# Kernel tuning notes

Hardware: AMD Instinct MI355X
Metric: run time of the kernel (lower is better)

The kernel has to match this reference:

```python
import jax, jax.numpy as jnp
import numpy as np
import math

GROUPS = 32
HEADS = 8
EPS = 1e-5


def group_norm(x, w, b):
    B, C, H, W = x.shape
    xg = x.reshape(B, GROUPS, C // GROUPS, H, W)
    mu = xg.mean(axis=(2, 3, 4), keepdims=True)
    var = xg.var(axis=(2, 3, 4), keepdims=True)
    xg = (xg - mu) * jax.lax.rsqrt(var + EPS)
    return xg.reshape(B, C, H, W) * w[None, :, None, None] + b[None, :, None, None]


def setup_inputs() -> dict:
    key = jax.random.key(0)
    ks = jax.random.split(key, 3)
    C = 512
    x = jax.random.normal(ks[0], (4, C, 64, 64), dtype=jnp.float32)
    norm_w = jnp.ones((C,), dtype=jnp.float32)
    norm_b = jnp.zeros((C,), dtype=jnp.float32)
    qkv_w = jax.random.normal(ks[1], (3 * C, C), dtype=jnp.float32) * 0.02
    qkv_b = jnp.zeros((3 * C,), dtype=jnp.float32)
    proj_w = jax.random.normal(ks[2], (C, C), dtype=jnp.float32) * 0.02
    proj_b = jnp.zeros((C,), dtype=jnp.float32)
    return {"x": x, "norm_w": norm_w, "norm_b": norm_b, "qkv_w": qkv_w,
            "qkv_b": qkv_b, "proj_w": proj_w, "proj_b": proj_b}


def reference(x, norm_w, norm_b, qkv_w, qkv_b, proj_w, proj_b):
    B, C, H, W = x.shape
    S = H * W
    head_dim = C // HEADS
    scale = 1.0 / math.sqrt(head_dim)

    h = group_norm(x, norm_w, norm_b)
    # 1x1 conv == pointwise linear over channels
    qkv = jnp.einsum('oc,bchw->bohw', qkv_w, h) + qkv_b[None, :, None, None]
    q, k, v = jnp.split(qkv, 3, axis=1)
    q = q.reshape(B, HEADS, head_dim, S)
    k = k.reshape(B, HEADS, head_dim, S)
    v = v.reshape(B, HEADS, head_dim, S)

    # chunked softmax attention in the original is row-wise softmax, i.e.
    # mathematically identical to full attention over all queries
    attn = jnp.einsum('bhdi,bhdj->bhij', q, k) * scale  # [B,H,S,S]
    attn = jax.nn.softmax(attn, axis=-1)
    out = jnp.einsum('bhij,bhdj->bhdi', attn, v)  # [B,H,d,S]

    out = out.reshape(B, C, H, W)
    out = jnp.einsum('oc,bchw->bohw', proj_w, out) + proj_b[None, :, None, None]
    return out + x
```

## Files before the change

kernel.cpp:

```cpp
#include <hip/hip_runtime.h>
#include <hip/hip_bf16.h>

#define NB 4
#define NC 512
#define NS 4096
#define NH 8
#define HD 64
#define NG 32
#define CPG 16
#define QKC 1024
#define CQF 0.18033688f

typedef __attribute__((ext_vector_type(8))) short bf16x8;
typedef __attribute__((ext_vector_type(4))) float f32x4;
typedef __attribute__((ext_vector_type(16))) float f32x16;

__device__ __forceinline__ unsigned short f2bf(float f) {
  union { float f; unsigned int u; } v; v.f = f;
  unsigned int r = v.u + 0x7FFFu + ((v.u >> 16) & 1u);
  return (unsigned short)(r >> 16);
}

__device__ __forceinline__ unsigned short f2bf_rn(float f) {
  union { __hip_bfloat16 h; unsigned short u; } cv;
  cv.h = __float2bfloat16(f);
  return cv.u;
}

__device__ __forceinline__ void gload16(const unsigned short* g, unsigned short* s) {
  __builtin_amdgcn_global_load_lds(
      (const __attribute__((address_space(1))) unsigned int*)g,
      (__attribute__((address_space(3))) unsigned int*)s, 16, 0, 0);
}

__global__ __launch_bounds__(256) void wprep_k(const float* __restrict__ wq,
                                               const float* __restrict__ wp,
                                               unsigned short* __restrict__ wqb,
                                               unsigned short* __restrict__ wpb,
                                               int nq8, int np8, int scale_end8) {
  int i = blockIdx.x * 256 + threadIdx.x;
  if (i >= nq8 + np8) return;
  const float* src;
  unsigned short* dst;
  float sc;
  int j;
  if (i < nq8) { src = wq; dst = wqb; j = i; sc = (i < scale_end8) ? CQF : 1.0f; }
  else         { src = wp; dst = wpb; j = i - nq8; sc = 1.0f; }
  const float4* s = (const float4*)src + (size_t)j * 2;
  float4 a = s[0], b = s[1];
  ushort4 u0 = make_ushort4(f2bf_rn(a.x * sc), f2bf_rn(a.y * sc),
                            f2bf_rn(a.z * sc), f2bf_rn(a.w * sc));
  ushort4 u1 = make_ushort4(f2bf_rn(b.x * sc), f2bf_rn(b.y * sc),
                            f2bf_rn(b.z * sc), f2bf_rn(b.w * sc));
  uint4 o;
  o.x = (unsigned)u0.x | ((unsigned)u0.y << 16);
  o.y = (unsigned)u0.z | ((unsigned)u0.w << 16);
  o.z = (unsigned)u1.x | ((unsigned)u1.y << 16);
  o.w = (unsigned)u1.z | ((unsigned)u1.w << 16);
  *((uint4*)dst + j) = o;
}

__global__ __launch_bounds__(256) void gn_stats_k(const float* __restrict__ x,
                                                  float* __restrict__ pstats) {
  int bgq = blockIdx.x;
  const float4* xp = (const float4*)(x + (size_t)bgq * (CPG * NS / 4));
  float s = 0.f, s2 = 0.f;
  #pragma unroll 4
  for (int i = threadIdx.x; i < CPG * NS / 16; i += 256) {
    float4 v = xp[i];
    s  += v.x + v.y + v.z + v.w;
    s2 += v.x * v.x + v.y * v.y + v.z * v.z + v.w * v.w;
  }
  #pragma unroll
  for (int off = 32; off > 0; off >>= 1) {
    s  += __shfl_down(s, off);
    s2 += __shfl_down(s2, off);
  }
  __shared__ float rs[4], rs2[4];
  int wid = threadIdx.x >> 6;
  if ((threadIdx.x & 63) == 0) { rs[wid] = s; rs2[wid] = s2; }
  __syncthreads();
  if (threadIdx.x == 0) {
    pstats[bgq * 2]     = rs[0] + rs[1] + rs[2] + rs[3];
    pstats[bgq * 2 + 1] = rs2[0] + rs2[1] + rs2[2] + rs2[3];
  }
}

__global__ __launch_bounds__(256) void gn_apply_k(const float* __restrict__ x,
                                                  const float* __restrict__ pstats,
                                                  const float* __restrict__ nw,
                                                  const float* __restrict__ nb,
                                                  unsigned short* __restrict__ ht) {
  int st = blockIdx.x, ct = blockIdx.y, b = blockIdx.z;
  int c0 = ct * 64, s0 = st * 64;
  __shared__ unsigned short lds[64][72];
  for (int idx = threadIdx.x; idx < 1024; idx += 256) {
    int row = idx >> 4, c4 = idx & 15;
    int c = c0 + row;
    int gi = (b * NG + (c >> 4)) * 4;
    const float4* pq = (const float4*)(pstats + gi * 2);
    float4 p01 = pq[0], p23 = pq[1];
    float sum = p01.x + p01.z + p23.x + p23.z;
    float ssq = p01.y + p01.w + p23.y + p23.w;
    float inv_n = 1.0f / (CPG * NS);
    float mu = sum * inv_n;
    float var = ssq * inv_n - mu * mu;
    float rstd = rsqrtf(var + 1e-5f);
    float sw = nw[c] * rstd;
    float sb = nb[c] - mu * sw;
    float4 v = *(const float4*)(x + ((size_t)b * NC + c) * NS + s0 + c4 * 4);
    ushort4 u = make_ushort4(f2bf(v.x * sw + sb), f2bf(v.y * sw + sb),
                             f2bf(v.z * sw + sb), f2bf(v.w * sw + sb));
    *(ushort4*)&lds[row][c4 * 4] = u;
  }
  __syncthreads();
  for (int idx = threadIdx.x; idx < 1024; idx += 256) {
    int i = idx >> 4, ch = idx & 15;
    ushort4 u = make_ushort4(lds[ch * 4 + 0][i], lds[ch * 4 + 1][i],
                             lds[ch * 4 + 2][i], lds[ch * 4 + 3][i]);
    *(ushort4*)(ht + ((size_t)b * NS + s0 + i) * NC + c0 + ch * 4) = u;
  }
}

__global__ __launch_bounds__(256) void qkv_gemm_k(const unsigned short* __restrict__ ht,
                                                  const unsigned short* __restrict__ wqb,
                                                  const float* __restrict__ bq,
                                                  unsigned short* __restrict__ qk,
                                                  unsigned short* __restrict__ vt) {
  int b = blockIdx.z;
  int m0 = blockIdx.x * 128, n0 = blockIdx.y * 128;
  __shared__ unsigned short alds[128 * 64];
  __shared__ unsigned short blds[128 * 64];
  const unsigned short* A = ht + (size_t)b * NS * NC;
  int tid = threadIdx.x;
  int l = tid & 63, w = tid >> 6;
  int wr = w >> 1, wc = w & 1;
  int lm = l & 15, lg = l >> 4;
  int lrow = l >> 3, lcb = l & 7;
  f32x4 acc[4][4];
  #pragma unroll
  for (int mi = 0; mi < 4; mi++)
    #pragma unroll
    for (int ni = 0; ni < 4; ni++) acc[mi][ni] = (f32x4){0.f, 0.f, 0.f, 0.f};

  for (int k0 = 0; k0 < NC; k0 += 64) {
    #pragma unroll
    for (int j = 0; j < 4; j++) {
      int row = w * 32 + j * 8 + lrow;
      int scb = lcb ^ (row & 7);
      gload16(A   + (size_t)(m0 + row) * NC + k0 + scb * 8, &alds[(w * 4 + j) * 512]);
      gload16(wqb + (size_t)(n0 + row) * NC + k0 + scb * 8, &blds[(w * 4 + j) * 512]);
    }
    __syncthreads();
    #pragma unroll
    for (int ks = 0; ks < 2; ks++) {
      bf16x8 af[4], bfr[4];
      #pragma unroll
      for (int mi = 0; mi < 4; mi++) {
        int row = wr * 64 + mi * 16 + lm;
        af[mi] = *(const bf16x8*)&alds[((row << 6) + (ks << 5) + (lg << 3)) ^ ((row & 7) << 3)];
      }
      #pragma unroll
      for (int ni = 0; ni < 4; ni++) {
        int row = wc * 64 + ni * 16 + lm;
        bfr[ni] = *(const bf16x8*)&blds[((row << 6) + (ks << 5) + (lg << 3)) ^ ((row & 7) << 3)];
      }
      #pragma unroll
      for (int mi = 0; mi < 4; mi++)
        #pragma unroll
        for (int ni = 0; ni < 4; ni++)
          acc[mi][ni] = __builtin_amdgcn_mfma_f32_16x16x32_bf16(af[mi], bfr[ni], acc[mi][ni], 0, 0, 0);
    }
    __syncthreads();
  }
  if (n0 < QKC) {
    #pragma unroll
    for (int mi = 0; mi < 4; mi++) {
      #pragma unroll
      for (int ni = 0; ni < 4; ni++) {
        int o = n0 + wc * 64 + ni * 16 + lm;
        float bias = bq[o];
        if (o < NC) bias *= CQF;
        #pragma unroll
        for (int q = 0; q < 4; q++) {
          int s = m0 + wr * 64 + mi * 16 + lg * 4 + q;
          qk[((size_t)b * NS + s) * QKC + o] = f2bf(acc[mi][ni][q] + bias);
        }
      }
    }
  } else {
    #pragma unroll
    for (int mi = 0; mi < 4; mi++) {
      int s0 = m0 + wr * 64 + mi * 16 + lg * 4;
      #pragma unroll
      for (int ni = 0; ni < 4; ni++) {
        int o = n0 + wc * 64 + ni * 16 + lm;
        float bias = bq[o];
        int dg = o - QKC;
        ushort4 u = make_ushort4(f2bf(acc[mi][ni][0] + bias), f2bf(acc[mi][ni][1] + bias),
                                 f2bf(acc[mi][ni][2] + bias), f2bf(acc[mi][ni][3] + bias));
        *(ushort4*)(vt + ((size_t)b * NC + dg) * NS + s0) = u;
      }
    }
  }
}

__global__ __launch_bounds__(256) void attn_k(const unsigned short* __restrict__ qk,
                                              const unsigned short* __restrict__ vt,
                                              unsigned short* __restrict__ ob) {
  int qt = blockIdx.x, h = blockIdx.y, b = blockIdx.z;
  int tid = threadIdx.x;
  int l = tid & 63, w = tid >> 6;
  int l31 = l & 31, hi = l >> 5;
  __shared__ unsigned short slds[16384];
  const unsigned short* qkb = qk + (size_t)b * NS * QKC;
  const unsigned short* vtb = vt + ((size_t)b * NC + h * HD) * NS;
  int iw = qt * 128 + w * 32;

  bf16x8 fq[4];
  #pragma unroll
  for (int kk = 0; kk < 4; kk++)
    fq[kk] = *(const bf16x8*)(qkb + (size_t)(iw + l31) * QKC + h * HD + kk * 16 + hi * 8);

  bf16x8 ones;
  #pragma unroll
  for (int e = 0; e < 8; e++) ones[e] = (short)0x3F80;

  int rb = (((l31 << 6) + (hi << 3)) ^ ((l31 & 7) << 3));
  int rbk[4] = { rb, rb ^ 16, rb ^ 32, rb ^ 48 };

  int sr = tid >> 3, sch = (tid & 7) * 8;
  const unsigned short* kp0 = qkb + NC + h * HD + (size_t)sr * QKC + sch;
  const unsigned short* kp1 = kp0 + (size_t)32 * QKC;
  const unsigned short* vp0 = vtb + (size_t)sr * NS + sch;
  const unsigned short* vp1 = vp0 + (size_t)32 * NS;
  int dk0 = (((sr << 6) + sch) ^ ((sr & 7) << 3));
  int dk1 = ((((sr + 32) << 6) + sch) ^ ((sr & 7) << 3));

  f32x16 acc_o0 = {}, acc_o1 = {}, acc_l = {};

  bf16x8 vA[8], vB[8], pA[4], pB[4];
  #pragma unroll
  for (int e = 0; e < 8; e++) vB[e] = (bf16x8){0, 0, 0, 0, 0, 0, 0, 0};
  #pragma unroll
  for (int e = 0; e < 4; e++) pB[e] = (bf16x8){0, 0, 0, 0, 0, 0, 0, 0};

  uint4 rk0 = *(const uint4*)kp0, rk1 = *(const uint4*)kp1;
  uint4 rv0 = *(const uint4*)vp0, rv1 = *(const uint4*)vp1;
  *(uint4*)&slds[dk0] = rk0;        *(uint4*)&slds[dk1] = rk1;
  *(uint4*)&slds[4096 + dk0] = rv0; *(uint4*)&slds[4096 + dk1] = rv1;
  kp0 += (size_t)64 * QKC; kp1 += (size_t)64 * QKC; vp0 += 64; vp1 += 64;
  rk0 = *(const uint4*)kp0; rk1 = *(const uint4*)kp1;
  rv0 = *(const uint4*)vp0; rv1 = *(const uint4*)vp1;
  __syncthreads();

  #define CVTSW(SA, q, DST) {                                                       \
    unsigned X0, X1, Y0, Y1;                                                        \
    asm("v_cvt_pk_bf16_f32 %0, %1, %2" : "=v"(X0) : "v"(SA[q*8+0]), "v"(SA[q*8+1]));\
    asm("v_cvt_pk_bf16_f32 %0, %1, %2" : "=v"(X1) : "v"(SA[q*8+2]), "v"(SA[q*8+3]));\
    asm("v_cvt_pk_bf16_f32 %0, %1, %2" : "=v"(Y0) : "v"(SA[q*8+4]), "v"(SA[q*8+5]));\
    asm("v_cvt_pk_bf16_f32 %0, %1, %2" : "=v"(Y1) : "v"(SA[q*8+6]), "v"(SA[q*8+7]));\
    asm("v_permlane32_swap_b32 %0, %1" : "+v"(X0), "+v"(Y0));                       \
    asm("v_permlane32_swap_b32 %0, %1" : "+v"(X1), "+v"(Y1));                       \
    union { unsigned u[4]; bf16x8 v; } pu = {{X0, X1, Y0, Y1}};                     \
    DST = pu.v; }

  #define TILE(BUF, t, VN, VP, PN, PP) {                                            \
    *(uint4*)&slds[(BUF^1)*8192 + dk0] = rk0;                                       \
    *(uint4*)&slds[(BUF^1)*8192 + dk1] = rk1;                                       \
    *(uint4*)&slds[(BUF^1)*8192 + 4096 + dk0] = rv0;                                \
    *(uint4*)&slds[(BUF^1)*8192 + 4096 + dk1] = rv1;                                \
    if ((t) + 2 < 64) {                                                             \
      kp0 += (size_t)64 * QKC; kp1 += (size_t)64 * QKC; vp0 += 64; vp1 += 64;       \
      rk0 = *(const uint4*)kp0; rk1 = *(const uint4*)kp1;                           \
      rv0 = *(const uint4*)vp0; rv1 = *(const uint4*)vp1;                           \
    }                                                                               \
    const unsigned short* Kr = &slds[(BUF)*8192];                                   \
    const unsigned short* Vr = &slds[(BUF)*8192 + 4096];                            \
    f32x16 sa0 = {}, sa1 = {};                                                      \
    __builtin_amdgcn_s_setprio(1);                                                  \
    _Pragma("unroll")                                                               \
    for (int kk = 0; kk < 4; kk++) {                                                \
      bf16x8 ak = *(const bf16x8*)&Kr[rbk[kk]];                                     \
      sa0 = __builtin_amdgcn_mfma_f32_32x32x16_bf16(ak, fq[kk], sa0, 0, 0, 0);      \
    }                                                                               \
    _Pragma("unroll")                                                               \
    for (int kk = 0; kk < 4; kk++) {                                                \
      bf16x8 ak = *(const bf16x8*)&Kr[rbk[kk] + 2048];                              \
      sa1 = __builtin_amdgcn_mfma_f32_32x32x16_bf16(ak, fq[kk], sa1, 0, 0, 0);      \
    }                                                                               \
    _Pragma("unroll")                                                               \
    for (int kk = 0; kk < 4; kk++) {                                                \
      VN[kk]     = *(const bf16x8*)&Vr[rbk[kk]];                                    \
      VN[kk + 4] = *(const bf16x8*)&Vr[rbk[kk] + 2048];                             \
    }                                                                               \
    _Pragma("unroll")                                                               \
    for (int bq_ = 0; bq_ < 4; bq_++) {                                             \
      acc_l  = __builtin_amdgcn_mfma_f32_32x32x16_bf16(PP[bq_], ones, acc_l, 0, 0, 0);        \
      acc_o0 = __builtin_amdgcn_mfma_f32_32x32x16_bf16(PP[bq_], VP[bq_], acc_o0, 0, 0, 0);    \
      acc_o1 = __builtin_amdgcn_mfma_f32_32x32x16_bf16(PP[bq_], VP[bq_ + 4], acc_o1, 0, 0, 0);\
    }                                                                               \
    __builtin_amdgcn_s_setprio(0);                                                  \
    _Pragma("unroll")                                                               \
    for (int r = 0; r < 16; r++) {                                                  \
      sa0[r] = __builtin_amdgcn_exp2f(sa0[r]);                                      \
      sa1[r] = __builtin_amdgcn_exp2f(sa1[r]);                                      \
    }                                                                               \
    CVTSW(sa0, 0, PN[0]);                                                           \
    CVTSW(sa0, 1, PN[1]);                                                           \
    CVTSW(sa1, 0, PN[2]);                                                           \
    CVTSW(sa1, 1, PN[3]);                                                           \
    __syncthreads(); }

  for (int t = 0; t < 64; t += 2) {
    TILE(0, t,     vA, vB, pA, pB)
    TILE(1, t + 1, vB, vA, pB, pA)
  }
  #undef TILE
  #undef CVTSW

  #pragma unroll
  for (int bq_ = 0; bq_ < 4; bq_++) {
    acc_l  = __builtin_amdgcn_mfma_f32_32x32x16_bf16(pB[bq_], ones, acc_l, 0, 0, 0);
    acc_o0 = __builtin_amdgcn_mfma_f32_32x32x16_bf16(pB[bq_], vB[bq_], acc_o0, 0, 0, 0);
    acc_o1 = __builtin_amdgcn_mfma_f32_32x32x16_bf16(pB[bq_], vB[bq_ + 4], acc_o1, 0, 0, 0);
  }

  #pragma unroll
  for (int r = 0; r < 16; r++) {
    float inv = __builtin_amdgcn_rcpf(acc_l[r]);
    int i = (r & 3) + 8 * (r >> 2) + 4 * hi;
    size_t rowo = ((size_t)b * NS + (iw + i)) * NC + h * HD;
    ob[rowo + l31]      = f2bf_rn(acc_o0[r] * inv);
    ob[rowo + 32 + l31] = f2bf_rn(acc_o1[r] * inv);
  }
}

__global__ __launch_bounds__(256) void proj_gemm_k(const unsigned short* __restrict__ wpb,
                                                   const float* __restrict__ bp,
                                                   const unsigned short* __restrict__ obuf,
                                                   const float* __restrict__ x,
                                                   float* __restrict__ out) {
  int b = blockIdx.z;
  int m0 = blockIdx.x * 128, n0 = blockIdx.y * 128;
  __shared__ unsigned short alds[128 * 64];
  __shared__ unsigned short blds[128 * 64];
  const unsigned short* Bt = obuf + (size_t)b * NS * NC;
  int tid = threadIdx.x;
  int l = tid & 63, w = tid >> 6;
  int wr = w >> 1, wc = w & 1;
  int lm = l & 15, lg = l >> 4;
  int lrow = l >> 3, lcb = l & 7;
  f32x4 acc[4][4];
  #pragma unroll
  for (int mi = 0; mi < 4; mi++)
    #pragma unroll
    for (int ni = 0; ni < 4; ni++) acc[mi][ni] = (f32x4){0.f, 0.f, 0.f, 0.f};

  for (int k0 = 0; k0 < NC; k0 += 64) {
    #pragma unroll
    for (int j = 0; j < 4; j++) {
      int row = w * 32 + j * 8 + lrow;
      int scb = lcb ^ (row & 7);
      gload16(wpb + (size_t)(m0 + row) * NC + k0 + scb * 8, &alds[(w * 4 + j) * 512]);
      gload16(Bt  + (size_t)(n0 + row) * NC + k0 + scb * 8, &blds[(w * 4 + j) * 512]);
    }
    __syncthreads();
    #pragma unroll
    for (int ks = 0; ks < 2; ks++) {
      bf16x8 af[4], bfr[4];
      #pragma unroll
      for (int mi = 0; mi < 4; mi++) {
        int row = wr * 64 + mi * 16 + lm;
        af[mi] = *(const bf16x8*)&alds[((row << 6) + (ks << 5) + (lg << 3)) ^ ((row & 7) << 3)];
      }
      #pragma unroll
      for (int ni = 0; ni < 4; ni++) {
        int row = wc * 64 + ni * 16 + lm;
        bfr[ni] = *(const bf16x8*)&blds[((row << 6) + (ks << 5) + (lg << 3)) ^ ((row & 7) << 3)];
      }
      #pragma unroll
      for (int mi = 0; mi < 4; mi++)
        #pragma unroll
        for (int ni = 0; ni < 4; ni++)
          acc[mi][ni] = __builtin_amdgcn_mfma_f32_16x16x32_bf16(af[mi], bfr[ni], acc[mi][ni], 0, 0, 0);
    }
    __syncthreads();
  }
  #pragma unroll
  for (int mi = 0; mi < 4; mi++) {
    #pragma unroll
    for (int q = 0; q < 4; q++) {
      int o = m0 + wr * 64 + mi * 16 + lg * 4 + q;
      float bias = bp[o];
      #pragma unroll
      for (int ni = 0; ni < 4; ni++) {
        int s = n0 + wc * 64 + ni * 16 + lm;
        size_t idx = ((size_t)b * NC + o) * NS + s;
        out[idx] = acc[mi][ni][q] + bias + x[idx];
      }
    }
  }
}

extern "C" void kernel_launch(void* const* d_in, const int* in_sizes, int n_in,
                              void* d_out, int out_size, void* d_ws, size_t ws_size,
                              hipStream_t stream) {
  const float* x  = (const float*)d_in[0];
  const float* nw = (const float*)d_in[1];
  const float* nb = (const float*)d_in[2];
  const float* wq = (const float*)d_in[3];
  const float* bq = (const float*)d_in[4];
  const float* wp = (const float*)d_in[5];
  const float* bp = (const float*)d_in[6];
  float* out = (float*)d_out;

  char* ws = (char*)d_ws;
  size_t off = 0;
  off += 1024;
  unsigned short* ht  = (unsigned short*)(ws + off); off += (size_t)NB * NS * NC * 2;
  unsigned short* qk  = (unsigned short*)(ws + off); off += (size_t)NB * NS * QKC * 2;
  unsigned short* vt  = (unsigned short*)(ws + off); off += (size_t)NB * NS * NC * 2;
  unsigned short* wqb = (unsigned short*)(ws + off); off += (size_t)3 * NC * NC * 2;
  unsigned short* wpb = (unsigned short*)(ws + off); off += (size_t)NC * NC * 2;
  unsigned short* ob  = ht;
  float* pstats = (float*)qk;

  const int nq8 = 3 * NC * NC / 8, np8 = NC * NC / 8;
  wprep_k<<<dim3((nq8 + np8 + 255) / 256), 256, 0, stream>>>(
      wq, wp, wqb, wpb, nq8, np8, NC * NC / 8);
  gn_stats_k<<<dim3(NB * NG * 4), 256, 0, stream>>>(x, pstats);
  gn_apply_k<<<dim3(NS / 64, NC / 64, NB), 256, 0, stream>>>(x, pstats, nw, nb, ht);
  qkv_gemm_k<<<dim3(NS / 128, 1536 / 128, NB), 256, 0, stream>>>(ht, wqb, bq, qk, vt);
  attn_k<<<dim3(NS / 128, NH, NB), 256, 0, stream>>>(qk, vt, ob);
  proj_gemm_k<<<dim3(NC / 128, NS / 128, NB), 256, 0, stream>>>(wpb, bp, ob, x, out);
}
```

Measured before the change: 246.7 us.

## Fuse prep kernels and restructure attention with 512-thread blocks and async LDS loads

Merges the weight-conversion and group-norm statistics kernels into one launch. The attention kernel grows to 512 threads covering 256 queries per block. Blocks are mapped so that each XCD handles whole (batch, head) pairs, improving L2 reuse of K/V. K/V tile staging moves from register round-trips to direct global-to-LDS loads, double-buffered with a vmcnt wait before each barrier. The risk is exposed load latency, because it waits for all loads at every tile, plus lower occupancy from the larger blocks.

```diff
diff --git a/kernel.cpp b/kernel.cpp
--- a/kernel.cpp
+++ b/kernel.cpp
@@ -33,56 +33,58 @@
       (__attribute__((address_space(3))) unsigned int*)s, 16, 0, 0);
 }
 
-__global__ __launch_bounds__(256) void wprep_k(const float* __restrict__ wq,
-                                               const float* __restrict__ wp,
-                                               unsigned short* __restrict__ wqb,
-                                               unsigned short* __restrict__ wpb,
-                                               int nq8, int np8, int scale_end8) {
-  int i = blockIdx.x * 256 + threadIdx.x;
-  if (i >= nq8 + np8) return;
-  const float* src;
-  unsigned short* dst;
-  float sc;
-  int j;
-  if (i < nq8) { src = wq; dst = wqb; j = i; sc = (i < scale_end8) ? CQF : 1.0f; }
-  else         { src = wp; dst = wpb; j = i - nq8; sc = 1.0f; }
-  const float4* s = (const float4*)src + (size_t)j * 2;
-  float4 a = s[0], b = s[1];
-  ushort4 u0 = make_ushort4(f2bf_rn(a.x * sc), f2bf_rn(a.y * sc),
-                            f2bf_rn(a.z * sc), f2bf_rn(a.w * sc));
-  ushort4 u1 = make_ushort4(f2bf_rn(b.x * sc), f2bf_rn(b.y * sc),
-                            f2bf_rn(b.z * sc), f2bf_rn(b.w * sc));
-  uint4 o;
-  o.x = (unsigned)u0.x | ((unsigned)u0.y << 16);
-  o.y = (unsigned)u0.z | ((unsigned)u0.w << 16);
-  o.z = (unsigned)u1.x | ((unsigned)u1.y << 16);
-  o.w = (unsigned)u1.z | ((unsigned)u1.w << 16);
-  *((uint4*)dst + j) = o;
-}
-
-__global__ __launch_bounds__(256) void gn_stats_k(const float* __restrict__ x,
-                                                  float* __restrict__ pstats) {
-  int bgq = blockIdx.x;
-  const float4* xp = (const float4*)(x + (size_t)bgq * (CPG * NS / 4));
-  float s = 0.f, s2 = 0.f;
-  #pragma unroll 4
-  for (int i = threadIdx.x; i < CPG * NS / 16; i += 256) {
-    float4 v = xp[i];
-    s  += v.x + v.y + v.z + v.w;
-    s2 += v.x * v.x + v.y * v.y + v.z * v.z + v.w * v.w;
-  }
-  #pragma unroll
-  for (int off = 32; off > 0; off >>= 1) {
-    s  += __shfl_down(s, off);
-    s2 += __shfl_down(s2, off);
-  }
-  __shared__ float rs[4], rs2[4];
-  int wid = threadIdx.x >> 6;
-  if ((threadIdx.x & 63) == 0) { rs[wid] = s; rs2[wid] = s2; }
-  __syncthreads();
-  if (threadIdx.x == 0) {
-    pstats[bgq * 2]     = rs[0] + rs[1] + rs[2] + rs[3];
-    pstats[bgq * 2 + 1] = rs2[0] + rs2[1] + rs2[2] + rs2[3];
+__global__ __launch_bounds__(256) void prep_k(const float* __restrict__ x,
+                                              float* __restrict__ pstats,
+                                              const float* __restrict__ wq,
+                                              const float* __restrict__ wp,
+                                              unsigned short* __restrict__ wqb,
+                                              unsigned short* __restrict__ wpb) {
+  int bid = blockIdx.x;
+  if (bid < NB * NG * 4) {
+    int bgq = bid;
+    const float4* xp = (const float4*)(x + (size_t)bgq * (CPG * NS / 4));
+    float s = 0.f, s2 = 0.f;
+    #pragma unroll 4
+    for (int i = threadIdx.x; i < CPG * NS / 16; i += 256) {
+      float4 v = xp[i];
+      s  += v.x + v.y + v.z + v.w;
+      s2 += v.x * v.x + v.y * v.y + v.z * v.z + v.w * v.w;
+    }
+    #pragma unroll
+    for (int off = 32; off > 0; off >>= 1) {
+      s  += __shfl_down(s, off);
+      s2 += __shfl_down(s2, off);
+    }
+    __shared__ float rs[4], rs2[4];
+    int wid = threadIdx.x >> 6;
+    if ((threadIdx.x & 63) == 0) { rs[wid] = s; rs2[wid] = s2; }
+    __syncthreads();
+    if (threadIdx.x == 0) {
+      pstats[bgq * 2]     = rs[0] + rs[1] + rs[2] + rs[3];
+      pstats[bgq * 2 + 1] = rs2[0] + rs2[1] + rs2[2] + rs2[3];
+    }
+  } else {
+    const int nq8 = 3 * NC * NC / 8, np8 = NC * NC / 8, se8 = NC * NC / 8;
+    int i = (bid - NB * NG * 4) * 256 + threadIdx.x;
+    if (i >= nq8 + np8) return;
+    const float* src;
+    unsigned short* dst;
+    float sc;
+    int j;
+    if (i < nq8) { src = wq; dst = wqb; j = i; sc = (i < se8) ? CQF : 1.0f; }
+    else         { src = wp; dst = wpb; j = i - nq8; sc = 1.0f; }
+    const float4* s = (const float4*)src + (size_t)j * 2;
+    float4 a = s[0], b = s[1];
+    ushort4 u0 = make_ushort4(f2bf_rn(a.x * sc), f2bf_rn(a.y * sc),
+                              f2bf_rn(a.z * sc), f2bf_rn(a.w * sc));
+    ushort4 u1 = make_ushort4(f2bf_rn(b.x * sc), f2bf_rn(b.y * sc),
+                              f2bf_rn(b.z * sc), f2bf_rn(b.w * sc));
+    uint4 o;
+    o.x = (unsigned)u0.x | ((unsigned)u0.y << 16);
+    o.y = (unsigned)u0.z | ((unsigned)u0.w << 16);
+    o.z = (unsigned)u1.x | ((unsigned)u1.y << 16);
+    o.w = (unsigned)u1.z | ((unsigned)u1.w << 16);
+    *((uint4*)dst + j) = o;
   }
 }
 
@@ -205,17 +207,21 @@
   }
 }
 
-__global__ __launch_bounds__(256) void attn_k(const unsigned short* __restrict__ qk,
+__global__ __launch_bounds__(512) void attn_k(const unsigned short* __restrict__ qk,
                                               const unsigned short* __restrict__ vt,
                                               unsigned short* __restrict__ ob) {
-  int qt = blockIdx.x, h = blockIdx.y, b = blockIdx.z;
+  int bid = blockIdx.x;
+  int xcd = bid & 7, g = bid >> 3;
+  int pair = xcd * 4 + (g >> 4);
+  int qt = g & 15;
+  int h = pair & 7, b = pair >> 3;
   int tid = threadIdx.x;
   int l = tid & 63, w = tid >> 6;
   int l31 = l & 31, hi = l >> 5;
   __shared__ unsigned short slds[16384];
   const unsigned short* qkb = qk + (size_t)b * NS * QKC;
   const unsigned short* vtb = vt + ((size_t)b * NC + h * HD) * NS;
-  int iw = qt * 128 + w * 32;
+  int iw = qt * 256 + w * 32;
 
   bf16x8 fq[4];
   #pragma unroll
@@ -229,13 +235,14 @@
   int rb = (((l31 << 6) + (hi << 3)) ^ ((l31 & 7) << 3));
   int rbk[4] = { rb, rb ^ 16, rb ^ 32, rb ^ 48 };
 
-  int sr = tid >> 3, sch = (tid & 7) * 8;
-  const unsigned short* kp0 = qkb + NC + h * HD + (size_t)sr * QKC + sch;
-  const unsigned short* kp1 = kp0 + (size_t)32 * QKC;
-  const unsigned short* vp0 = vtb + (size_t)sr * NS + sch;
-  const unsigned short* vp1 = vp0 + (size_t)32 * NS;
-  int dk0 = (((sr << 6) + sch) ^ ((sr & 7) << 3));
-  int dk1 = ((((sr + 32) << 6) + sch) ^ ((sr & 7) << 3));
+  int kr = w * 8 + (l >> 3);
+  int scb = (l & 7) ^ (l >> 3);
+  const unsigned short* kgp = qkb + NC + h * HD + (size_t)kr * QKC + scb * 8;
+  const unsigned short* vgp = vtb + (size_t)kr * NS + scb * 8;
+  unsigned short* kdA = &slds[w * 512];
+  unsigned short* kdB = &slds[8192 + w * 512];
+  unsigned short* vdA = &slds[4096 + w * 512];
+  unsigned short* vdB = &slds[12288 + w * 512];
 
   f32x16 acc_o0 = {}, acc_o1 = {}, acc_l = {};
 
@@ -245,13 +252,10 @@
   #pragma unroll
   for (int e = 0; e < 4; e++) pB[e] = (bf16x8){0, 0, 0, 0, 0, 0, 0, 0};
 
-  uint4 rk0 = *(const uint4*)kp0, rk1 = *(const uint4*)kp1;
-  uint4 rv0 = *(const uint4*)vp0, rv1 = *(const uint4*)vp1;
-  *(uint4*)&slds[dk0] = rk0;        *(uint4*)&slds[dk1] = rk1;
-  *(uint4*)&slds[4096 + dk0] = rv0; *(uint4*)&slds[4096 + dk1] = rv1;
-  kp0 += (size_t)64 * QKC; kp1 += (size_t)64 * QKC; vp0 += 64; vp1 += 64;
-  rk0 = *(const uint4*)kp0; rk1 = *(const uint4*)kp1;
-  rv0 = *(const uint4*)vp0; rv1 = *(const uint4*)vp1;
+  gload16(kgp, kdA);
+  gload16(vgp, vdA);
+  kgp += (size_t)64 * QKC; vgp += 64;
+  asm volatile("s_waitcnt vmcnt(0)" ::: "memory");
   __syncthreads();
 
   #define CVTSW(SA, q, DST) {                                                       \
@@ -265,15 +269,11 @@
     union { unsigned u[4]; bf16x8 v; } pu = {{X0, X1, Y0, Y1}};                     \
     DST = pu.v; }
 
-  #define TILE(BUF, t, VN, VP, PN, PP) {                                            \
-    *(uint4*)&slds[(BUF^1)*8192 + dk0] = rk0;                                       \
-    *(uint4*)&slds[(BUF^1)*8192 + dk1] = rk1;                                       \
-    *(uint4*)&slds[(BUF^1)*8192 + 4096 + dk0] = rv0;                                \
-    *(uint4*)&slds[(BUF^1)*8192 + 4096 + dk1] = rv1;                                \
-    if ((t) + 2 < 64) {                                                             \
-      kp0 += (size_t)64 * QKC; kp1 += (size_t)64 * QKC; vp0 += 64; vp1 += 64;       \
-      rk0 = *(const uint4*)kp0; rk1 = *(const uint4*)kp1;                           \
-      rv0 = *(const uint4*)vp0; rv1 = *(const uint4*)vp1;                           \
+  #define TILE(BUF, t, VN, VP, PN, PP, KD, VD) {                                    \
+    if ((t) + 1 < 64) {                                                             \
+      gload16(kgp, KD);                                                             \
+      gload16(vgp, VD);                                                             \
+      kgp += (size_t)64 * QKC; vgp += 64;                                           \
     }                                                                               \
     const unsigned short* Kr = &slds[(BUF)*8192];                                   \
     const unsigned short* Vr = &slds[(BUF)*8192 + 4096];                            \
@@ -310,11 +310,12 @@
     CVTSW(sa0, 1, PN[1]);                                                           \
     CVTSW(sa1, 0, PN[2]);                                                           \
     CVTSW(sa1, 1, PN[3]);                                                           \
+    asm volatile("s_waitcnt vmcnt(0)" ::: "memory");                                \
     __syncthreads(); }
 
   for (int t = 0; t < 64; t += 2) {
-    TILE(0, t,     vA, vB, pA, pB)
-    TILE(1, t + 1, vB, vA, pB, pA)
+    TILE(0, t,     vA, vB, pA, pB, kdB, vdB)
+    TILE(1, t + 1, vB, vA, pB, pA, kdA, vdA)
   }
   #undef TILE
   #undef CVTSW
@@ -426,12 +427,9 @@
   unsigned short* ob  = ht;
   float* pstats = (float*)qk;
 
-  const int nq8 = 3 * NC * NC / 8, np8 = NC * NC / 8;
-  wprep_k<<<dim3((nq8 + np8 + 255) / 256), 256, 0, stream>>>(
-      wq, wp, wqb, wpb, nq8, np8, NC * NC / 8);
-  gn_stats_k<<<dim3(NB * NG * 4), 256, 0, stream>>>(x, pstats);
+  prep_k<<<dim3(1024), 256, 0, stream>>>(x, pstats, wq, wp, wqb, wpb);
   gn_apply_k<<<dim3(NS / 64, NC / 64, NB), 256, 0, stream>>>(x, pstats, nw, nb, ht);
   qkv_gemm_k<<<dim3(NS / 128, 1536 / 128, NB), 256, 0, stream>>>(ht, wqb, bq, qk, vt);
-  attn_k<<<dim3(NS / 128, NH, NB), 256, 0, stream>>>(qk, vt, ob);
+  attn_k<<<dim3(512), 512, 0, stream>>>(qk, vt, ob);
   proj_gemm_k<<<dim3(NC / 128, NS / 128, NB), 256, 0, stream>>>(wpb, bp, ob, x, out);
 }
```

Result: faster. 219.6 us, median of 2 (-11.0%).
